# Kernel optimization log

Measured on AMD Instinct MI355X. Metric: run time of the kernel, lower is better.

The kernel has to match this reference:

```python
import jax, jax.numpy as jnp
import numpy as np

B, S, D = 2, 2048, 4096
H, KVH, HD = 32, 8, 128
REPEATS = H // KVH
SCALE = HD ** -0.5


def setup_inputs() -> dict:
    key = jax.random.key(0)
    ks = jax.random.split(key, 5)
    x = jax.random.normal(ks[0], (B, S, D), dtype=jnp.float32)
    # RoPE tables: shape (S, HD//2)
    t = jnp.arange(S, dtype=jnp.float32)
    inv_freq = 1.0 / (10000.0 ** (jnp.arange(0, HD, 2, dtype=jnp.float32) / HD))
    freqs = jnp.outer(t, inv_freq)
    freqs_cos = jnp.cos(freqs)
    freqs_sin = jnp.sin(freqs)
    # causal additive mask [B, S, S]
    i = jnp.arange(S)
    causal = jnp.where(i[:, None] >= i[None, :], 0.0, -1e9).astype(jnp.float32)
    mask = jnp.broadcast_to(causal[None], (B, S, S))
    positions = jnp.arange(S, dtype=jnp.int32)
    w_std = 0.02
    wq = jax.random.normal(ks[1], (D, H * HD), dtype=jnp.float32) * w_std
    wk = jax.random.normal(ks[2], (D, KVH * HD), dtype=jnp.float32) * w_std
    wv = jax.random.normal(ks[3], (D, KVH * HD), dtype=jnp.float32) * w_std
    wo = jax.random.normal(ks[4], (H * HD, D), dtype=jnp.float32) * w_std
    return dict(x=x, freqs_cos=freqs_cos, freqs_sin=freqs_sin, mask=mask,
                wq=wq, wk=wk, wv=wv, wo=wo, positions=positions)


def _apply_rope(t, fc, fs):
    # t: [B, S, h, HD]; interleaved (real, imag) pairs along last dim
    tr = t.reshape(t.shape[:-1] + (HD // 2, 2))
    r, i = tr[..., 0], tr[..., 1]
    c = fc[None, :, None, :]  # [1, S, 1, HD//2]
    s = fs[None, :, None, :]
    out_r = r * c - i * s
    out_i = r * s + i * c
    return jnp.stack([out_r, out_i], axis=-1).reshape(t.shape)


def reference(x, freqs_cos, freqs_sin, mask, wq, wk, wv, wo, positions):
    bsz, seqlen, _ = x.shape
    xq = (x @ wq).reshape(bsz, seqlen, H, HD)
    xk = (x @ wk).reshape(bsz, seqlen, KVH, HD)
    xv = (x @ wv).reshape(bsz, seqlen, KVH, HD)
    xq = _apply_rope(xq, freqs_cos, freqs_sin)
    xk = _apply_rope(xk, freqs_cos, freqs_sin)
    # GQA: repeat_interleave over kv-head dim
    key = jnp.repeat(xk, REPEATS, axis=2)   # [B, S, H, HD]
    value = jnp.repeat(xv, REPEATS, axis=2)
    q = xq.transpose(0, 2, 1, 3)            # [B, H, S, HD]
    k = key.transpose(0, 2, 1, 3)
    v = value.transpose(0, 2, 1, 3)
    scores = jnp.einsum('bhqd,bhkd->bhqk', q, k) * SCALE
    scores = scores + mask[:, None, :, :]
    probs = jax.nn.softmax(scores.astype(jnp.float32), axis=-1)
    out = jnp.einsum('bhqk,bhkd->bhqd', probs, v)
    out = out.transpose(0, 2, 1, 3).reshape(bsz, seqlen, H * HD)
    out = jnp.nan_to_num(out)
    return out @ wo
```

## Files before the change

### kernel.cpp

```cpp
#include <hip/hip_runtime.h>

typedef unsigned short ushort_t;
typedef unsigned int uint32;

#define SCALE_F 0.08838834764831845f

using bf16x8 = __attribute__((ext_vector_type(8))) short;
using f32x4  = __attribute__((ext_vector_type(4))) float;
using u32x4  = __attribute__((ext_vector_type(4))) uint32;
using u32x2  = __attribute__((ext_vector_type(2))) uint32;

__device__ __forceinline__ float b2f(ushort_t h) {
  union { uint32 u; float f; } v; v.u = ((uint32)h) << 16; return v.f;
}
__device__ __forceinline__ ushort_t f2b(float f) {
  union { float f; uint32 u; } v; v.f = f;
  uint32 r = (v.u + 0x7fffu + ((v.u >> 16) & 1u)) >> 16;
  return (ushort_t)r;
}
__device__ __forceinline__ uint32 pk2(float a, float b) {
  union { float f; uint32 u; } x, y; x.f = a; y.f = b;
  return __builtin_amdgcn_perm(y.u + 0x8000u, x.u + 0x8000u, 0x07060302u);
}
__device__ __forceinline__ void gl2lds16(const void* g, void* l) {
  __builtin_amdgcn_global_load_lds(
      (const __attribute__((address_space(1))) uint32*)g,
      (__attribute__((address_space(3))) uint32*)l, 16, 0, 0);
}
__device__ __forceinline__ void fence_mem() { asm volatile("" ::: "memory"); }
__device__ __forceinline__ void bar() {
  fence_mem();
  __builtin_amdgcn_s_barrier();
  fence_mem();
}
template <int N>
__device__ __forceinline__ void waitvm() {
  if constexpr (N == 6) asm volatile("s_waitcnt vmcnt(6)" ::: "memory");
  else if constexpr (N == 8) asm volatile("s_waitcnt vmcnt(8)" ::: "memory");
  else asm volatile("s_waitcnt vmcnt(0)" ::: "memory");
}

constexpr int LDP = 40;


__global__ __launch_bounds__(256)
void xconv(const float* __restrict__ x, ushort_t* __restrict__ xb) {
  size_t i = ((size_t)blockIdx.x * 256 + threadIdx.x) * 8;
  f32x4 a = *(const f32x4*)&x[i];
  f32x4 b = *(const f32x4*)&x[i + 4];
  u32x4 p = {pk2(a[0], a[1]), pk2(a[2], a[3]), pk2(b[0], b[1]), pk2(b[2], b[3])};
  *(u32x4*)&xb[i] = p;
}

__global__ __launch_bounds__(256)
void wtrans(const float* __restrict__ src, ushort_t* __restrict__ dst, int N) {
  __shared__ float ts[32][33];
  int n0 = blockIdx.x * 32, k0 = blockIdx.y * 32;
  int tid = threadIdx.x;
  {
    int r = tid >> 3, c4 = (tid & 7) * 4;
    f32x4 v = *(const f32x4*)&src[(size_t)(k0 + r) * N + n0 + c4];
    ts[r][c4 + 0] = v[0]; ts[r][c4 + 1] = v[1];
    ts[r][c4 + 2] = v[2]; ts[r][c4 + 3] = v[3];
  }
  __syncthreads();
  int rn = tid >> 3, ck = (tid & 7) * 4;
  u32x2 p = {pk2(ts[ck + 0][rn], ts[ck + 1][rn]),
             pk2(ts[ck + 2][rn], ts[ck + 3][rn])};
  *(u32x2*)&dst[(size_t)(n0 + rn) * 4096 + k0 + ck] = p;
}


template <int ROWS, int AMODE>
__device__ __forceinline__ void stage_region(const ushort_t* __restrict__ P,
                                             int row0, int k, ushort_t* lds,
                                             int tid) {
#pragma unroll
  for (int i = 0; i < ROWS / 128; ++i) {
    int s = i * 512 + tid;
    int r = s >> 2, c = s & 3;
    int qq = c ^ ((r >> 1) & 3);
    const ushort_t* ga;
    if (AMODE == 0) {
      ga = P + (size_t)(row0 + r) * 4096 + k + qq * 8;
    } else {
      int m = row0 + r, bb = m >> 11, ss = m & 2047;
      int kk = k + qq * 8;
      int hh = kk >> 7, dg = (kk >> 5) & 3;
      ga = P + ((((size_t)(bb * 32 + hh) * 32 + (ss >> 6)) * 4 + dg) * 64 +
                (ss & 63)) * 32 + (kk & 31);
    }
    gl2lds16(ga, lds + ((size_t)(i * 512 + (tid & 448))) * 8);
  }
}

template <int BM, int AMODE>
__device__ __forceinline__ void gemm8p_core(const ushort_t* __restrict__ A,
                                            const ushort_t* __restrict__ B,
                                            int m0, int n0, ushort_t* As,
                                            ushort_t* Bs, f32x4 (*acc)[4]) {
  constexpr int FR = BM / 32;
  constexpr int ASZ = BM * 32;
  constexpr int BSZ = 256 * 32;
  constexpr int SPP = BM / 128 + 2;
  constexpr int VMC = 2 * SPP;
  const int tid = threadIdx.x;
  const int lane = tid & 63, q = lane >> 4, cl = lane & 15;
  const int w = tid >> 6, wrow = w >> 2, wcol = w & 3;

  auto stage_pair = [&](int pl, int k) {
    stage_region<BM, AMODE>(A, m0, k, As + pl * ASZ, tid);
    stage_region<256, 0>(B, n0, k, Bs + pl * BSZ, tid);
  };

  stage_pair(0, 0);
  stage_pair(1, 32);
  stage_pair(2, 64);
  waitvm<VMC>();
  bar();

  for (int t = 0; t < 128; ++t) {
    int pl = t & 3;
    int kf = (t + 3) * 32; if (kf > 4064) kf = 4064;
    const ushort_t* ap = As + pl * ASZ;
    const ushort_t* bp = Bs + pl * BSZ;
    bf16x8 af[FR], bfr[4];
#pragma unroll
    for (int fr = 0; fr < FR; ++fr) {
      int rr = wrow * (BM / 2) + fr * 16 + cl;
      af[fr] = *(const bf16x8*)&ap[rr * 32 + (q ^ ((rr >> 1) & 3)) * 8];
    }
#pragma unroll
    for (int fb = 0; fb < 4; ++fb) {
      int rn = wcol * 64 + fb * 16 + cl;
      bfr[fb] = *(const bf16x8*)&bp[rn * 32 + (q ^ ((rn >> 1) & 3)) * 8];
    }
    stage_pair((t + 3) & 3, kf);
    bar();
    __builtin_amdgcn_s_setprio(1);
#pragma unroll
    for (int fr = 0; fr < FR; ++fr)
#pragma unroll
      for (int fb = 0; fb < 4; ++fb)
        acc[fr][fb] = __builtin_amdgcn_mfma_f32_16x16x32_bf16(
            af[fr], bfr[fb], acc[fr][fb], 0, 0, 0);
    __builtin_amdgcn_s_setprio(0);
    waitvm<VMC>();
    bar();
  }
  waitvm<0>();
  bar();
}

__global__ __launch_bounds__(512, 2)
void qkv_gemm8(const ushort_t* __restrict__ xb, const ushort_t* __restrict__ wt,
               const float* __restrict__ fc, const float* __restrict__ fs,
               ushort_t* __restrict__ qg, ushort_t* __restrict__ kg,
               ushort_t* __restrict__ vg) {
  __shared__ ushort_t As[4 * 128 * 32];
  __shared__ ushort_t Bs[4 * 256 * 32];
  int bid = blockIdx.x;
  int swz = (bid & 7) * 96 + (bid >> 3);
  int tx = swz / 32, ty = swz % 32;
  int n0 = tx * 256, m0 = ty * 128;
  f32x4 acc[4][4] = {};
  gemm8p_core<128, 0>(xb, wt, m0, n0, As, Bs, acc);
  const int tid = threadIdx.x;
  const int lane = tid & 63, q = lane >> 4, cl = lane & 15;
  const int w = tid >> 6, wrow = w >> 2, wcol = w & 3;
  if (n0 < 5120) {
    ushort_t* dst = (n0 < 4096) ? qg : kg;
    int NHH = (n0 < 4096) ? 32 : 8;
    int nc = (n0 < 4096) ? n0 : n0 - 4096;
    for (int fr = 0; fr < 4; ++fr)
      for (int fcc = 0; fcc < 4; ++fcc)
        for (int rg = 0; rg < 4; ++rg) {
          int row = m0 + wrow * 64 + fr * 16 + q * 4 + rg;
          int b = row >> 11, s = row & 2047;
          int col = nc + wcol * 64 + fcc * 16 + cl;
          int hh = col >> 7, d = col & 127;
          float val = acc[fr][fcc][rg];
          float par = __shfl_xor(val, 1);
          float cf = fc[(size_t)s * 64 + (d >> 1)];
          float sf = fs[(size_t)s * 64 + (d >> 1)];
          float o = val * cf + par * ((d & 1) ? sf : -sf);
          size_t off =
              ((((size_t)(b * NHH + hh) * 32 + (s >> 6)) * 4 + (d >> 5)) * 64 +
               (s & 63)) * 32 + (d & 31);
          dst[off] = f2b(o);
        }
  } else {
    int nc = n0 - 5120;
    for (int fr = 0; fr < 4; ++fr)
      for (int fcc = 0; fcc < 4; ++fcc)
        for (int rg = 0; rg < 4; ++rg) {
          int row = m0 + wrow * 64 + fr * 16 + q * 4 + rg;
          int b = row >> 11, s = row & 2047;
          int col = nc + wcol * 64 + fcc * 16 + cl;
          int kvh = col >> 7, d = col & 127;
          size_t off =
              ((((size_t)(b * 8 + kvh) * 32 + (s >> 6)) * 2 + ((s >> 5) & 1)) *
                   128 + d) * 32 + (s & 31);
          vg[off] = f2b(acc[fr][fcc][rg]);
        }
  }
}

__global__ __launch_bounds__(512, 2)
void out_gemm8(const ushort_t* __restrict__ attn,
               const ushort_t* __restrict__ wot, float* __restrict__ out) {
  __shared__ ushort_t As[4 * 256 * 32];
  __shared__ ushort_t Bs[4 * 256 * 32];
  int bid = blockIdx.x;
  int swz = (bid & 7) * 32 + (bid >> 3);
  int tx = swz >> 4, ty = swz & 15;
  int n0 = tx * 256, m0 = ty * 256;
  f32x4 acc[8][4] = {};
  gemm8p_core<256, 1>(attn, wot, m0, n0, As, Bs, acc);
  const int tid = threadIdx.x;
  const int lane = tid & 63, q = lane >> 4, cl = lane & 15;
  const int w = tid >> 6, wrow = w >> 2, wcol = w & 3;
  for (int fr = 0; fr < 8; ++fr)
    for (int fcc = 0; fcc < 4; ++fcc)
      for (int rg = 0; rg < 4; ++rg) {
        int row = m0 + wrow * 128 + fr * 16 + q * 4 + rg;
        int col = n0 + wcol * 64 + fcc * 16 + cl;
        out[(size_t)row * 4096 + col] = acc[fr][fcc][rg];
      }
}


template <int AMODE>
__device__ __forceinline__ void gemm_core_cvt(const void* __restrict__ A,
                                              const float* __restrict__ B, int K,
                                              int NB, int m0, int nb0,
                                              ushort_t* As, ushort_t* Bs,
                                              f32x4 acc[4][4]) {
  int tid = threadIdx.x;
  int lane = tid & 63, w = tid >> 6, q = lane >> 4, cl = lane & 15;
  int wr = (w >> 1) * 64, wc = (w & 1) * 64;
  int ar = tid >> 1, ah = tid & 1;
  int bn = tid & 127, bh = tid >> 7;
  for (int k0 = 0; k0 < K; k0 += 32) {
    __syncthreads();
    if (AMODE == 0) {
      const float* ap = &((const float*)A)[(size_t)(m0 + ar) * K + k0 + ah * 16];
      f32x4 a0 = *(const f32x4*)(ap + 0);
      f32x4 a1 = *(const f32x4*)(ap + 4);
      f32x4 a2 = *(const f32x4*)(ap + 8);
      f32x4 a3 = *(const f32x4*)(ap + 12);
      u32x4 p0 = {pk2(a0[0], a0[1]), pk2(a0[2], a0[3]), pk2(a1[0], a1[1]),
                  pk2(a1[2], a1[3])};
      u32x4 p1 = {pk2(a2[0], a2[1]), pk2(a2[2], a2[3]), pk2(a3[0], a3[1]),
                  pk2(a3[2], a3[3])};
      *(u32x4*)&As[ar * LDP + ah * 16] = p0;
      *(u32x4*)&As[ar * LDP + ah * 16 + 8] = p1;
    } else {
      int m = m0 + ar, bb = m >> 11, s = m & 2047;
      int k = k0 + ah * 16;
      int hh = k >> 7, dg = (k >> 5) & 3, el = k & 31;
      size_t off =
          ((((size_t)(bb * 32 + hh) * 32 + (s >> 6)) * 4 + dg) * 64 +
           (s & 63)) * 32 + el;
      const ushort_t* ap = (const ushort_t*)A + off;
      u32x4 v0 = *(const u32x4*)(ap + 0);
      u32x4 v1 = *(const u32x4*)(ap + 8);
      *(u32x4*)&As[ar * LDP + ah * 16] = v0;
      *(u32x4*)&As[ar * LDP + ah * 16 + 8] = v1;
    }
    {
      float bv[16];
#pragma unroll
      for (int j = 0; j < 16; ++j)
        bv[j] = B[(size_t)(k0 + bh * 16 + j) * NB + nb0 + bn];
      u32x4 p0 = {pk2(bv[0], bv[1]), pk2(bv[2], bv[3]), pk2(bv[4], bv[5]),
                  pk2(bv[6], bv[7])};
      u32x4 p1 = {pk2(bv[8], bv[9]), pk2(bv[10], bv[11]), pk2(bv[12], bv[13]),
                  pk2(bv[14], bv[15])};
      *(u32x4*)&Bs[bn * LDP + bh * 16] = p0;
      *(u32x4*)&Bs[bn * LDP + bh * 16 + 8] = p1;
    }
    __syncthreads();
    bf16x8 af[4], bfr[4];
    for (int rt = 0; rt < 4; ++rt)
      af[rt] = *(const bf16x8*)&As[(wr + rt * 16 + cl) * LDP + q * 8];
    for (int ct = 0; ct < 4; ++ct)
      bfr[ct] = *(const bf16x8*)&Bs[(wc + ct * 16 + cl) * LDP + q * 8];
    for (int rt = 0; rt < 4; ++rt)
      for (int ct = 0; ct < 4; ++ct)
        acc[rt][ct] = __builtin_amdgcn_mfma_f32_16x16x32_bf16(
            af[rt], bfr[ct], acc[rt][ct], 0, 0, 0);
  }
}

__global__ __launch_bounds__(256, 3)
void qkv_gemm_cvt(const float* __restrict__ x, const float* __restrict__ wq,
                  const float* __restrict__ wk, const float* __restrict__ wv,
                  const float* __restrict__ fc, const float* __restrict__ fs,
                  ushort_t* __restrict__ qg, ushort_t* __restrict__ kg,
                  ushort_t* __restrict__ vg) {
  __shared__ ushort_t As[128 * LDP];
  __shared__ ushort_t Bs[128 * LDP];
  int n0 = blockIdx.x * 128, m0 = blockIdx.y * 128;
  const float* Bp; int NB, nc;
  if (n0 < 4096)      { Bp = wq; NB = 4096; nc = n0; }
  else if (n0 < 5120) { Bp = wk; NB = 1024; nc = n0 - 4096; }
  else                { Bp = wv; NB = 1024; nc = n0 - 5120; }
  f32x4 acc[4][4] = {};
  gemm_core_cvt<0>(x, Bp, 4096, NB, m0, nc, As, Bs, acc);
  int tid = threadIdx.x;
  int lane = tid & 63, w = tid >> 6, q = lane >> 4, cl = lane & 15;
  int wr = (w >> 1) * 64, wc = (w & 1) * 64;
  if (n0 < 5120) {
    ushort_t* dst = (n0 < 4096) ? qg : kg;
    int NHH = (n0 < 4096) ? 32 : 8;
    for (int rt = 0; rt < 4; ++rt)
      for (int ct = 0; ct < 4; ++ct)
        for (int rg = 0; rg < 4; ++rg) {
          int row = m0 + wr + rt * 16 + q * 4 + rg;
          int b = row >> 11, s = row & 2047;
          int col = nc + wc + ct * 16 + cl;
          int hh = col >> 7, d = col & 127;
          float val = acc[rt][ct][rg];
          float par = __shfl_xor(val, 1);
          float cf = fc[(size_t)s * 64 + (d >> 1)];
          float sf = fs[(size_t)s * 64 + (d >> 1)];
          float o = val * cf + par * ((d & 1) ? sf : -sf);
          size_t off =
              ((((size_t)(b * NHH + hh) * 32 + (s >> 6)) * 4 + (d >> 5)) * 64 +
               (s & 63)) * 32 + (d & 31);
          dst[off] = f2b(o);
        }
  } else {
    for (int rt = 0; rt < 4; ++rt)
      for (int ct = 0; ct < 4; ++ct)
        for (int rg = 0; rg < 4; ++rg) {
          int row = m0 + wr + rt * 16 + q * 4 + rg;
          int b = row >> 11, s = row & 2047;
          int col = nc + wc + ct * 16 + cl;
          int kvh = col >> 7, d = col & 127;
          size_t off =
              ((((size_t)(b * 8 + kvh) * 32 + (s >> 6)) * 2 + ((s >> 5) & 1)) *
                   128 + d) * 32 + (s & 31);
          vg[off] = f2b(acc[rt][ct][rg]);
        }
  }
}

__global__ __launch_bounds__(256, 3)
void out_gemm_cvt(const ushort_t* __restrict__ attn,
                  const float* __restrict__ wo, float* __restrict__ out) {
  __shared__ ushort_t As[128 * LDP];
  __shared__ ushort_t Bs[128 * LDP];
  int n0 = blockIdx.x * 128, m0 = blockIdx.y * 128;
  f32x4 acc[4][4] = {};
  gemm_core_cvt<1>(attn, wo, 4096, 4096, m0, n0, As, Bs, acc);
  int tid = threadIdx.x;
  int lane = tid & 63, w = tid >> 6, q = lane >> 4, cl = lane & 15;
  int wr = (w >> 1) * 64, wc = (w & 1) * 64;
  for (int rt = 0; rt < 4; ++rt)
    for (int ct = 0; ct < 4; ++ct)
      for (int rg = 0; rg < 4; ++rg) {
        int row = m0 + wr + rt * 16 + q * 4 + rg;
        int col = n0 + wc + ct * 16 + cl;
        out[(size_t)row * 4096 + col] = acc[rt][ct][rg];
      }
}

__device__ __forceinline__ void stage_tile(const ushort_t* src, ushort_t* dst,
                                           int tid) {
  for (int cc = 0; cc < 4; ++cc)
    gl2lds16(src + (size_t)(cc * 256 + tid) * 8,
             dst + (size_t)(cc * 256 + (tid & 192)) * 8);
}

__global__ __launch_bounds__(256, 2)
void flash_attn(ushort_t* __restrict__ qg, const ushort_t* __restrict__ kg,
                const ushort_t* __restrict__ vg) {
  __shared__ ushort_t Ks[2][8192];
  __shared__ ushort_t Vs[2][8192];
  __shared__ ushort_t Ps[4096];
  int tid = threadIdx.x;
  int w = tid >> 6, lane = tid & 63, q = lane >> 4, cl = lane & 15;
  int idx = blockIdx.x;
  int qb = 31 - (idx >> 6);
  int bh = idx & 63;
  int b = bh >> 5, h = bh & 31, kvh = h >> 2;

  ushort_t* qt = qg + ((size_t)(b * 32 + h) * 32 + qb) * 8192;
  bf16x8 aq[4];
  for (int ks = 0; ks < 4; ++ks)
    aq[ks] = *(const bf16x8*)&qt[ks * 2048 + (w * 16 + cl) * 32 + q * 8];

  const ushort_t* kb = kg + ((size_t)(b * 8 + kvh) * 32) * 8192;
  const ushort_t* vb = vg + ((size_t)(b * 8 + kvh) * 32) * 8192;
  stage_tile(kb, Ks[0], tid);
  stage_tile(vb, Vs[0], tid);

  f32x4 oacc[8] = {};
  float m_i[4], l_i[4];
  for (int rg = 0; rg < 4; ++rg) { m_i[rg] = -3e30f; l_i[rg] = 0.f; }

  for (int jb = 0; jb <= qb; ++jb) {
    __syncthreads();
    int cur = jb & 1, nxt = (jb + 1) & 1;
    int jn = (jb + 1 > qb) ? qb : jb + 1;
    stage_tile(kb + (size_t)jn * 8192, Ks[nxt], tid);
    stage_tile(vb + (size_t)jn * 8192, Vs[nxt], tid);
    f32x4 sacc[4] = {};
    for (int ks = 0; ks < 4; ++ks)
      for (int ct = 0; ct < 4; ++ct) {
        bf16x8 bk =
            *(const bf16x8*)&Ks[cur][ks * 2048 + (ct * 16 + cl) * 32 + q * 8];
        sacc[ct] =
            __builtin_amdgcn_mfma_f32_16x16x32_bf16(aq[ks], bk, sacc[ct], 0, 0, 0);
      }
    float pv[4][4], mt[4];
    bool diag = (jb == qb);
    for (int rg = 0; rg < 4; ++rg) mt[rg] = -3e30f;
    for (int ct = 0; ct < 4; ++ct)
      for (int rg = 0; rg < 4; ++rg) {
        float sv = sacc[ct][rg] * SCALE_F;
        if (diag) {
          int rrow = w * 16 + q * 4 + rg;
          int ccol = ct * 16 + cl;
          if (ccol > rrow) sv = -3e30f;
        }
        pv[ct][rg] = sv;
        mt[rg] = fmaxf(mt[rg], sv);
      }
    for (int off = 1; off < 16; off <<= 1)
      for (int rg = 0; rg < 4; ++rg)
        mt[rg] = fmaxf(mt[rg], __shfl_xor(mt[rg], off));
    float alpha[4], rs[4];
    for (int rg = 0; rg < 4; ++rg) {
      float mn = fmaxf(m_i[rg], mt[rg]);
      alpha[rg] = __expf(m_i[rg] - mn);
      m_i[rg] = mn;
      rs[rg] = 0.f;
    }
    for (int ct = 0; ct < 4; ++ct)
      for (int rg = 0; rg < 4; ++rg) {
        float p = __expf(pv[ct][rg] - m_i[rg]);
        pv[ct][rg] = p;
        rs[rg] += p;
      }
    for (int off = 1; off < 16; off <<= 1)
      for (int rg = 0; rg < 4; ++rg) rs[rg] += __shfl_xor(rs[rg], off);
    for (int rg = 0; rg < 4; ++rg) l_i[rg] = l_i[rg] * alpha[rg] + rs[rg];
    for (int nt = 0; nt < 8; ++nt)
      for (int rg = 0; rg < 4; ++rg) oacc[nt][rg] *= alpha[rg];
    for (int ct = 0; ct < 4; ++ct)
      for (int rg = 0; rg < 4; ++rg) {
        int off_ = w * 1024 + (ct >> 1) * 512 + (q * 4 + rg) * 32 +
                   (ct & 1) * 16 + cl;
        Ps[off_] = f2b(pv[ct][rg]);
      }
    for (int ks2 = 0; ks2 < 2; ++ks2) {
      bf16x8 pa = *(const bf16x8*)&Ps[w * 1024 + ks2 * 512 + cl * 32 + q * 8];
      for (int nt = 0; nt < 8; ++nt) {
        bf16x8 bv =
            *(const bf16x8*)&Vs[cur][ks2 * 4096 + (nt * 16 + cl) * 32 + q * 8];
        oacc[nt] =
            __builtin_amdgcn_mfma_f32_16x16x32_bf16(pa, bv, oacc[nt], 0, 0, 0);
      }
    }
  }
  for (int nt = 0; nt < 8; ++nt)
    for (int rg = 0; rg < 4; ++rg) {
      float v = oacc[nt][rg] / l_i[rg];
      int rowt = w * 16 + q * 4 + rg;
      int d = nt * 16 + cl;
      qt[(d >> 5) * 2048 + rowt * 32 + (d & 31)] = f2b(v);
    }
}

extern "C" void kernel_launch(void* const* d_in, const int* in_sizes, int n_in,
                              void* d_out, int out_size, void* d_ws,
                              size_t ws_size, hipStream_t stream) {
  const float* x  = (const float*)d_in[0];
  const float* fc = (const float*)d_in[1];
  const float* fs = (const float*)d_in[2];
  const float* wq = (const float*)d_in[4];
  const float* wk = (const float*)d_in[5];
  const float* wv = (const float*)d_in[6];
  const float* wo = (const float*)d_in[7];
  ushort_t* ws = (ushort_t*)d_ws;

  ushort_t* qg = ws;
  ushort_t* kg = qg + (size_t)4096 * 4096;
  ushort_t* vg = kg + (size_t)4096 * 1024;

  if (ws_size >= (size_t)128 * 1024 * 1024) {
    ushort_t* wt = vg + (size_t)4096 * 1024;
    ushort_t* xb = wt + (size_t)6144 * 4096;
    xconv<<<8192, 256, 0, stream>>>(x, xb);
    wtrans<<<dim3(128, 128), 256, 0, stream>>>(wq, wt, 4096);
    wtrans<<<dim3(32, 128), 256, 0, stream>>>(wk, wt + (size_t)4096 * 4096, 1024);
    wtrans<<<dim3(32, 128), 256, 0, stream>>>(wv, wt + (size_t)5120 * 4096, 1024);
    qkv_gemm8<<<768, 512, 0, stream>>>(xb, wt, fc, fs, qg, kg, vg);
    wtrans<<<dim3(128, 128), 256, 0, stream>>>(wo, xb, 4096);
    flash_attn<<<2048, 256, 0, stream>>>(qg, kg, vg);
    out_gemm8<<<256, 512, 0, stream>>>(qg, xb, (float*)d_out);
  } else {
    qkv_gemm_cvt<<<dim3(48, 32), 256, 0, stream>>>(x, wq, wk, wv, fc, fs, qg,
                                                   kg, vg);
    flash_attn<<<2048, 256, 0, stream>>>(qg, kg, vg);
    out_gemm_cvt<<<dim3(32, 32), 256, 0, stream>>>(qg, wo, (float*)d_out);
  }
}
```

Before: 786.9 us.

## Restructure GEMM mainloop to K=64 steps with triple buffering, shrink out-proj tile

The shared GEMM core now advances K by 64 per iteration (two 32-wide halves) using a 3-slot ring buffer instead of 32 per step with a 4-slot ring. That halves the barriers per K, and the next stage is issued before the fragment reads. The output projection drops from 256x256 tiles to 128x256 tiles, doubling its grid to 512 blocks for better CU occupancy on 256 CUs. In exchange there are more register fragments per step, an explicit lgkmcnt wait, and less reuse per tile in the out-projection.

```diff
diff --git a/kernel.cpp b/kernel.cpp
--- a/kernel.cpp
+++ b/kernel.cpp
@@ -38,6 +38,9 @@
   if constexpr (N == 6) asm volatile("s_waitcnt vmcnt(6)" ::: "memory");
   else if constexpr (N == 8) asm volatile("s_waitcnt vmcnt(8)" ::: "memory");
   else asm volatile("s_waitcnt vmcnt(0)" ::: "memory");
+}
+__device__ __forceinline__ void waitlgkm0() {
+  asm volatile("s_waitcnt lgkmcnt(0)" ::: "memory");
 }
 
 constexpr int LDP = 40;
@@ -94,58 +97,64 @@
   }
 }
 
-template <int BM, int AMODE>
-__device__ __forceinline__ void gemm8p_core(const ushort_t* __restrict__ A,
+template <int AMODE>
+__device__ __forceinline__ void gemm64_core(const ushort_t* __restrict__ A,
                                             const ushort_t* __restrict__ B,
                                             int m0, int n0, ushort_t* As,
                                             ushort_t* Bs, f32x4 (*acc)[4]) {
-  constexpr int FR = BM / 32;
-  constexpr int ASZ = BM * 32;
-  constexpr int BSZ = 256 * 32;
-  constexpr int SPP = BM / 128 + 2;
-  constexpr int VMC = 2 * SPP;
+  constexpr int AKH = 128 * 32;
+  constexpr int BKH = 256 * 32;
   const int tid = threadIdx.x;
   const int lane = tid & 63, q = lane >> 4, cl = lane & 15;
   const int w = tid >> 6, wrow = w >> 2, wcol = w & 3;
 
-  auto stage_pair = [&](int pl, int k) {
-    stage_region<BM, AMODE>(A, m0, k, As + pl * ASZ, tid);
-    stage_region<256, 0>(B, n0, k, Bs + pl * BSZ, tid);
+  auto stage_buf = [&](int b, int k) {
+    stage_region<128, AMODE>(A, m0, k,      As + b * 2 * AKH, tid);
+    stage_region<128, AMODE>(A, m0, k + 32, As + b * 2 * AKH + AKH, tid);
+    stage_region<256, 0>(B, n0, k,      Bs + b * 2 * BKH, tid);
+    stage_region<256, 0>(B, n0, k + 32, Bs + b * 2 * BKH + BKH, tid);
   };
 
-  stage_pair(0, 0);
-  stage_pair(1, 32);
-  stage_pair(2, 64);
-  waitvm<VMC>();
+  stage_buf(0, 0);
+  stage_buf(1, 64);
+  waitvm<6>();
   bar();
 
-  for (int t = 0; t < 128; ++t) {
-    int pl = t & 3;
-    int kf = (t + 3) * 32; if (kf > 4064) kf = 4064;
-    const ushort_t* ap = As + pl * ASZ;
-    const ushort_t* bp = Bs + pl * BSZ;
-    bf16x8 af[FR], bfr[4];
-#pragma unroll
-    for (int fr = 0; fr < FR; ++fr) {
-      int rr = wrow * (BM / 2) + fr * 16 + cl;
-      af[fr] = *(const bf16x8*)&ap[rr * 32 + (q ^ ((rr >> 1) & 3)) * 8];
-    }
-#pragma unroll
-    for (int fb = 0; fb < 4; ++fb) {
-      int rn = wcol * 64 + fb * 16 + cl;
-      bfr[fb] = *(const bf16x8*)&bp[rn * 32 + (q ^ ((rn >> 1) & 3)) * 8];
-    }
-    stage_pair((t + 3) & 3, kf);
-    bar();
+  for (int t = 0; t < 64; ++t) {
+    int b = t % 3;
+    int k2 = t + 2; if (k2 > 63) k2 = 63;
+    const ushort_t* ap = As + b * 2 * AKH;
+    const ushort_t* bp = Bs + b * 2 * BKH;
+    stage_buf((t + 2) % 3, k2 * 64);
+    bf16x8 af[2][4], bfr[2][4];
+#pragma unroll
+    for (int h = 0; h < 2; ++h)
+#pragma unroll
+      for (int fr = 0; fr < 4; ++fr) {
+        int rr = wrow * 64 + fr * 16 + cl;
+        af[h][fr] =
+            *(const bf16x8*)&ap[h * AKH + rr * 32 + (q ^ ((rr >> 1) & 3)) * 8];
+      }
+#pragma unroll
+    for (int h = 0; h < 2; ++h)
+#pragma unroll
+      for (int fb = 0; fb < 4; ++fb) {
+        int rn = wcol * 64 + fb * 16 + cl;
+        bfr[h][fb] =
+            *(const bf16x8*)&bp[h * BKH + rn * 32 + (q ^ ((rn >> 1) & 3)) * 8];
+      }
     __builtin_amdgcn_s_setprio(1);
 #pragma unroll
-    for (int fr = 0; fr < FR; ++fr)
-#pragma unroll
-      for (int fb = 0; fb < 4; ++fb)
-        acc[fr][fb] = __builtin_amdgcn_mfma_f32_16x16x32_bf16(
-            af[fr], bfr[fb], acc[fr][fb], 0, 0, 0);
+    for (int h = 0; h < 2; ++h)
+#pragma unroll
+      for (int fr = 0; fr < 4; ++fr)
+#pragma unroll
+        for (int fb = 0; fb < 4; ++fb)
+          acc[fr][fb] = __builtin_amdgcn_mfma_f32_16x16x32_bf16(
+              af[h][fr], bfr[h][fb], acc[fr][fb], 0, 0, 0);
     __builtin_amdgcn_s_setprio(0);
-    waitvm<VMC>();
+    waitlgkm0();
+    waitvm<6>();
     bar();
   }
   waitvm<0>();
@@ -157,14 +166,14 @@
                const float* __restrict__ fc, const float* __restrict__ fs,
                ushort_t* __restrict__ qg, ushort_t* __restrict__ kg,
                ushort_t* __restrict__ vg) {
-  __shared__ ushort_t As[4 * 128 * 32];
-  __shared__ ushort_t Bs[4 * 256 * 32];
+  __shared__ ushort_t As[3 * 2 * 128 * 32];
+  __shared__ ushort_t Bs[3 * 2 * 256 * 32];
   int bid = blockIdx.x;
   int swz = (bid & 7) * 96 + (bid >> 3);
   int tx = swz / 32, ty = swz % 32;
   int n0 = tx * 256, m0 = ty * 128;
   f32x4 acc[4][4] = {};
-  gemm8p_core<128, 0>(xb, wt, m0, n0, As, Bs, acc);
+  gemm64_core<0>(xb, wt, m0, n0, As, Bs, acc);
   const int tid = threadIdx.x;
   const int lane = tid & 63, q = lane >> 4, cl = lane & 15;
   const int w = tid >> 6, wrow = w >> 2, wcol = w & 3;
@@ -209,21 +218,21 @@
 __global__ __launch_bounds__(512, 2)
 void out_gemm8(const ushort_t* __restrict__ attn,
                const ushort_t* __restrict__ wot, float* __restrict__ out) {
-  __shared__ ushort_t As[4 * 256 * 32];
-  __shared__ ushort_t Bs[4 * 256 * 32];
+  __shared__ ushort_t As[3 * 2 * 128 * 32];
+  __shared__ ushort_t Bs[3 * 2 * 256 * 32];
   int bid = blockIdx.x;
-  int swz = (bid & 7) * 32 + (bid >> 3);
-  int tx = swz >> 4, ty = swz & 15;
-  int n0 = tx * 256, m0 = ty * 256;
-  f32x4 acc[8][4] = {};
-  gemm8p_core<256, 1>(attn, wot, m0, n0, As, Bs, acc);
+  int swz = (bid & 7) * 64 + (bid >> 3);
+  int tx = swz >> 5, ty = swz & 31;
+  int n0 = tx * 256, m0 = ty * 128;
+  f32x4 acc[4][4] = {};
+  gemm64_core<1>(attn, wot, m0, n0, As, Bs, acc);
   const int tid = threadIdx.x;
   const int lane = tid & 63, q = lane >> 4, cl = lane & 15;
   const int w = tid >> 6, wrow = w >> 2, wcol = w & 3;
-  for (int fr = 0; fr < 8; ++fr)
+  for (int fr = 0; fr < 4; ++fr)
     for (int fcc = 0; fcc < 4; ++fcc)
       for (int rg = 0; rg < 4; ++rg) {
-        int row = m0 + wrow * 128 + fr * 16 + q * 4 + rg;
+        int row = m0 + wrow * 64 + fr * 16 + q * 4 + rg;
         int col = n0 + wcol * 64 + fcc * 16 + cl;
         out[(size_t)row * 4096 + col] = acc[fr][fcc][rg];
       }
@@ -501,7 +510,7 @@
     qkv_gemm8<<<768, 512, 0, stream>>>(xb, wt, fc, fs, qg, kg, vg);
     wtrans<<<dim3(128, 128), 256, 0, stream>>>(wo, xb, 4096);
     flash_attn<<<2048, 256, 0, stream>>>(qg, kg, vg);
-    out_gemm8<<<256, 512, 0, stream>>>(qg, xb, (float*)d_out);
+    out_gemm8<<<512, 512, 0, stream>>>(qg, xb, (float*)d_out);
   } else {
     qkv_gemm_cvt<<<dim3(48, 32), 256, 0, stream>>>(x, wq, wk, wv, fc, fs, qg,
                                                    kg, vg);
```

Result: slower. 911.1 us (+15.8%).
